# Performance work log

Hardware: AMD Instinct MI355X
Metric: run time of the kernel (lower is better)

Reference implementation:

```python
import jax, jax.numpy as jnp
import numpy as np

N = 50000   # nodes
E = 640000  # edges
IN = 256    # in_dim
H = 128     # hidden
OUT = 40    # out_dim
EPS = 1e-5  # BatchNorm eps


def setup_inputs() -> dict:
    key = jax.random.key(0)
    ks = jax.random.split(key, 14)
    x = jax.random.normal(ks[0], (N, IN), jnp.float32)
    edge_index = jax.random.randint(ks[1], (2, E), 0, N)
    def lin(k, fan_in, shape):
        return jax.random.normal(k, shape, jnp.float32) / np.float32(np.sqrt(fan_in))
    return {
        "x": x,
        "edge_index": edge_index,
        # block 0 (256 -> 128, has res_proj)
        "W0": lin(ks[2], IN, (IN, H)),
        "b0": jnp.zeros((H,), jnp.float32),
        "g0": jnp.ones((H,), jnp.float32),
        "be0": jnp.zeros((H,), jnp.float32),
        "pW": lin(ks[3], IN, (IN, H)),
        "pb": jnp.zeros((H,), jnp.float32),
        # block 1 (128 -> 128, identity residual)
        "W1": lin(ks[4], H, (H, H)),
        "b1": jnp.zeros((H,), jnp.float32),
        "g1": jnp.ones((H,), jnp.float32),
        "be1": jnp.zeros((H,), jnp.float32),
        # head
        "hW": lin(ks[5], H, (H, OUT)),
        "hb": jnp.zeros((OUT,), jnp.float32),
    }


def _gcn_conv(x, W, b, edge_index):
    """GCNConv(improved=True): x' = D^-1/2 (A + 2I) D^-1/2 (x W) + b."""
    h = x @ W  # [N, dout]
    row, col = edge_index[0], edge_index[1]  # source -> target
    # degree of A + 2I (edge_weight = 1, self-loop fill = 2.0)
    deg = jnp.zeros((N,), h.dtype).at[col].add(1.0) + 2.0
    dis = jax.lax.rsqrt(deg)  # deg > 0 always (self-loops)
    norm = dis[row] * dis[col]  # [E]
    # neighbor aggregation: scatter-add normalized messages to targets
    agg = jnp.zeros_like(h).at[col].add(norm[:, None] * h[row])
    # self-loop contribution with weight 2.0
    agg = agg + (2.0 * dis * dis)[:, None] * h
    return agg + b


def _bn(x, gamma, beta):
    # batch statistics (training-mode BatchNorm math), biased variance
    m = jnp.mean(x, axis=0)
    v = jnp.mean(jnp.square(x - m), axis=0)
    return (x - m) * jax.lax.rsqrt(v + EPS) * gamma + beta


def reference(x, edge_index, W0, b0, g0, be0, pW, pb, W1, b1, g1, be1, hW, hb):
    # block 0: conv -> bn -> relu -> (+ res_proj(x))
    out = jax.nn.relu(_bn(_gcn_conv(x, W0, b0, edge_index), g0, be0))
    x1 = out + (x @ pW + pb)
    # block 1: conv -> bn -> relu -> (+ identity)
    out = jax.nn.relu(_bn(_gcn_conv(x1, W1, b1, edge_index), g1, be1))
    x2 = out + x1
    return x2 @ hW + hb  # [N, OUT]
```

## Files before the change

kernel.cpp:

```cpp
#include <hip/hip_runtime.h>

#define H 128
#define IN_DIM 256
#define OUT_DIM 40
#define EPS 1e-5f

typedef unsigned short ushortT;
typedef __attribute__((ext_vector_type(8))) short bf16x8;
typedef __attribute__((ext_vector_type(4))) float f32x4;

static __device__ __forceinline__ ushortT f2bf(float f) {
    union { float f; unsigned u; } v; v.f = f;
    unsigned r = v.u + 0x7FFF + ((v.u >> 16) & 1);
    return (ushortT)(r >> 16);
}
static __device__ __forceinline__ unsigned pk2(float a, float b) {
    return (unsigned)f2bf(a) | ((unsigned)f2bf(b) << 16);
}
static __device__ __forceinline__ float bflo(unsigned v) {
    union { unsigned u; float f; } t; t.u = v << 16; return t.f;
}
static __device__ __forceinline__ float bfhi(unsigned v) {
    union { unsigned u; float f; } t; t.u = v & 0xFFFF0000u; return t.f;
}


__global__ __launch_bounds__(256) void count_kernel(const int* __restrict__ ei, int E, int* __restrict__ cnt) {
    int e = blockIdx.x * 256 + threadIdx.x;
    if (e < E) atomicAdd(&cnt[ei[E + e]], 1);
}

__global__ __launch_bounds__(256) void scan_block_sum(const int* __restrict__ cnt, int* __restrict__ bsum,
                                                      float* __restrict__ dis, int N) {
    __shared__ int s[256];
    int i = blockIdx.x * 256 + threadIdx.x;
    int v = (i < N) ? cnt[i] : 0;
    if (i < N) dis[i] = rsqrtf((float)v + 2.0f);
    s[threadIdx.x] = v;
    __syncthreads();
    for (int o = 128; o > 0; o >>= 1) {
        if (threadIdx.x < o) s[threadIdx.x] += s[threadIdx.x + o];
        __syncthreads();
    }
    if (threadIdx.x == 0) bsum[blockIdx.x] = s[0];
}

__global__ void scan_tops(const int* __restrict__ bsum, int* __restrict__ boff, int* __restrict__ rowptrN, int nb) {
    __shared__ int s[256];
    int t = threadIdx.x;
    int v = (t < nb) ? bsum[t] : 0;
    s[t] = v;
    __syncthreads();
    for (int o = 1; o < 256; o <<= 1) {
        int u = (t >= o) ? s[t - o] : 0;
        __syncthreads();
        s[t] += u;
        __syncthreads();
    }
    if (t < nb) boff[t] = s[t] - v;
    if (t == 255) *rowptrN = s[255];
}

__global__ __launch_bounds__(256) void scan_final(const int* __restrict__ cnt, const int* __restrict__ boff,
                                                  int* __restrict__ rowptr, int* __restrict__ cursor, int N) {
    __shared__ int s[256];
    int t = threadIdx.x;
    int i = blockIdx.x * 256 + t;
    int v = (i < N) ? cnt[i] : 0;
    s[t] = v;
    __syncthreads();
    for (int o = 1; o < 256; o <<= 1) {
        int u = (t >= o) ? s[t - o] : 0;
        __syncthreads();
        s[t] += u;
        __syncthreads();
    }
    if (i < N) {
        int e = boff[blockIdx.x] + s[t] - v;
        rowptr[i] = e;
        cursor[i] = e;
    }
}

__global__ __launch_bounds__(256) void fill_xcd(const int* __restrict__ ei, int E, int nper,
                                                int* __restrict__ cursor, int* __restrict__ eidx) {
    int xcd = blockIdx.x & 7;
    int nchunk = gridDim.x >> 3;
    int chunk = blockIdx.x >> 3;
    int csz = (E + nchunk - 1) / nchunk;
    int beg = chunk * csz;
    int end = min(E, beg + csz);
    for (int e = beg + (int)threadIdx.x; e < end; e += 256) {
        int c = ei[E + e];
        if (c / nper == xcd) {
            int slot = atomicAdd(&cursor[c], 1);
            eidx[slot] = ei[e];
        }
    }
}


__global__ __launch_bounds__(256) void prep_weights(const float* __restrict__ W0, const float* __restrict__ pW,
                                                    const float* __restrict__ W1, const float* __restrict__ hW,
                                                    ushortT* __restrict__ Wt0, ushortT* __restrict__ WtP,
                                                    ushortT* __restrict__ Wt1, ushortT* __restrict__ WtH) {
    int i = blockIdx.x * 256 + threadIdx.x;
    if (i < 32768) { int n = i >> 8, k = i & 255; Wt0[i] = f2bf(W0[k * 128 + n]); WtP[i] = f2bf(pW[k * 128 + n]); }
    if (i < 16384) { int n = i >> 7, k = i & 127; Wt1[i] = f2bf(W1[k * 128 + n]); }
    if (i < 6144)  { int n = i >> 7, k = i & 127; WtH[i] = (n < OUT_DIM) ? f2bf(hW[k * OUT_DIM + n]) : (ushortT)0; }
}


__global__ __launch_bounds__(512) void mgemm0(const float* __restrict__ X,
                                              const ushortT* __restrict__ Wt0,
                                              const ushortT* __restrict__ WtP,
                                              const float* __restrict__ pb,
                                              ushortT* __restrict__ Oh,
                                              ushortT* __restrict__ Op,
                                              int N) {
    __shared__ __align__(16) ushortT S[17408];
    int tid = threadIdx.x;
    int brow = blockIdx.x * 64;

#pragma unroll
    for (int i = 0; i < 8; ++i) {
        int idx = i * 512 + tid;
        int row = idx >> 6, c4 = idx & 63;
        int gr = brow + row;
        float4 v = make_float4(0.f, 0.f, 0.f, 0.f);
        if (gr < N) v = *(const float4*)&X[(size_t)gr * IN_DIM + c4 * 4];
        uint2 p;
        p.x = pk2(v.x, v.y);
        p.y = pk2(v.z, v.w);
        *(uint2*)&S[row * 264 + c4 * 4] = p;
    }
    __syncthreads();

    int w = tid >> 6, lane = tid & 63;
    int lm = lane & 15, lk = lane >> 4;
    int mat = w >> 2;
    int colbase = (w & 3) * 32;
    const ushortT* Wt = mat ? WtP : Wt0;

    f32x4 acc[4][2];
#pragma unroll
    for (int mt = 0; mt < 4; ++mt)
#pragma unroll
        for (int nt = 0; nt < 2; ++nt) acc[mt][nt] = (f32x4)0.f;

#pragma unroll
    for (int kc = 0; kc < 2; ++kc) {
        bf16x8 breg[2][4];
#pragma unroll
        for (int nt = 0; nt < 2; ++nt)
#pragma unroll
            for (int ks = 0; ks < 4; ++ks)
                breg[nt][ks] = *(const bf16x8*)&Wt[(size_t)(colbase + nt * 16 + lm) * IN_DIM + kc * 128 + ks * 32 + lk * 8];
#pragma unroll
        for (int ks = 0; ks < 4; ++ks) {
            bf16x8 af[4];
#pragma unroll
            for (int mt = 0; mt < 4; ++mt)
                af[mt] = *(const bf16x8*)&S[(mt * 16 + lm) * 264 + kc * 128 + ks * 32 + lk * 8];
#pragma unroll
            for (int nt = 0; nt < 2; ++nt)
#pragma unroll
                for (int mt = 0; mt < 4; ++mt)
                    acc[mt][nt] = __builtin_amdgcn_mfma_f32_16x16x32_bf16(af[mt], breg[nt][ks], acc[mt][nt], 0, 0, 0);
        }
    }

    float bb[2] = {0.f, 0.f};
    if (mat) {
        bb[0] = pb[colbase + lm];
        bb[1] = pb[colbase + 16 + lm];
    }
    __syncthreads();
#pragma unroll
    for (int mt = 0; mt < 4; ++mt)
#pragma unroll
        for (int nt = 0; nt < 2; ++nt) {
            int col = colbase + nt * 16 + lm;
#pragma unroll
            for (int j = 0; j < 4; ++j) {
                int row = mt * 16 + lk * 4 + j;
                S[mat * 8704 + row * 136 + col] = f2bf(acc[mt][nt][j] + bb[nt]);
            }
        }
    __syncthreads();
#pragma unroll
    for (int i = 0; i < 4; ++i) {
        int idx = i * 512 + tid;
        int m2 = idx >> 10;
        int rem = idx & 1023;
        int row = rem >> 4, colq = rem & 15;
        int gr = brow + row;
        if (gr < N) {
            uint4 v = *(const uint4*)&S[m2 * 8704 + row * 136 + colq * 8];
            ushortT* O = m2 ? Op : Oh;
            *(uint4*)&O[(size_t)gr * 128 + colq * 8] = v;
        }
    }
}


__global__ __launch_bounds__(512) void mgemm1_fused(const uint4* __restrict__ aggb,
                                                    const uint4* __restrict__ projb,
                                                    const float* __restrict__ stats,
                                                    const float* __restrict__ g,
                                                    const float* __restrict__ be,
                                                    const ushortT* __restrict__ Wt1,
                                                    ushortT* __restrict__ O,
                                                    uint4* __restrict__ x1b,
                                                    int N) {
    __shared__ __align__(16) ushortT S[17408];
    __shared__ float sc[128], sh[128];
    int tid = threadIdx.x;
    int brow = blockIdx.x * 128;

    if (tid < 128) {
        float mean = stats[tid] / (float)N;
        float var = stats[128 + tid] / (float)N - mean * mean;
        float inv = rsqrtf(var + EPS);
        float s = g[tid] * inv;
        sc[tid] = s;
        sh[tid] = be[tid] - mean * s;
    }
    __syncthreads();

#pragma unroll
    for (int i = 0; i < 4; ++i) {
        int idx = i * 512 + tid;
        int row = idx >> 4, q = idx & 15;
        int gr = brow + row;
        uint4 a = make_uint4(0u, 0u, 0u, 0u), p = a;
        if (gr < N) {
            size_t gidx = (size_t)gr * 16 + q;
            a = aggb[gidx];
            p = projb[gidx];
        }
        int ch = q * 8;
        float v0 = fmaxf(fmaf(bflo(a.x), sc[ch + 0], sh[ch + 0]), 0.f) + bflo(p.x);
        float v1 = fmaxf(fmaf(bfhi(a.x), sc[ch + 1], sh[ch + 1]), 0.f) + bfhi(p.x);
        float v2 = fmaxf(fmaf(bflo(a.y), sc[ch + 2], sh[ch + 2]), 0.f) + bflo(p.y);
        float v3 = fmaxf(fmaf(bfhi(a.y), sc[ch + 3], sh[ch + 3]), 0.f) + bfhi(p.y);
        float v4 = fmaxf(fmaf(bflo(a.z), sc[ch + 4], sh[ch + 4]), 0.f) + bflo(p.z);
        float v5 = fmaxf(fmaf(bfhi(a.z), sc[ch + 5], sh[ch + 5]), 0.f) + bfhi(p.z);
        float v6 = fmaxf(fmaf(bflo(a.w), sc[ch + 6], sh[ch + 6]), 0.f) + bflo(p.w);
        float v7 = fmaxf(fmaf(bfhi(a.w), sc[ch + 7], sh[ch + 7]), 0.f) + bfhi(p.w);
        uint4 pv;
        pv.x = pk2(v0, v1);
        pv.y = pk2(v2, v3);
        pv.z = pk2(v4, v5);
        pv.w = pk2(v6, v7);
        *(uint4*)&S[row * 136 + q * 8] = pv;
        if (gr < N) x1b[(size_t)gr * 16 + q] = pv;
    }
    __syncthreads();

    int w = tid >> 6, lane = tid & 63;
    int lm = lane & 15, lk = lane >> 4;
    int rh = (w >> 2) * 64;
    int colbase = (w & 3) * 32;

    bf16x8 breg[2][4];
#pragma unroll
    for (int nt = 0; nt < 2; ++nt)
#pragma unroll
        for (int ks = 0; ks < 4; ++ks)
            breg[nt][ks] = *(const bf16x8*)&Wt1[(size_t)(colbase + nt * 16 + lm) * H + ks * 32 + lk * 8];

    f32x4 acc[4][2];
#pragma unroll
    for (int mt = 0; mt < 4; ++mt)
#pragma unroll
        for (int nt = 0; nt < 2; ++nt) acc[mt][nt] = (f32x4)0.f;

#pragma unroll
    for (int ks = 0; ks < 4; ++ks) {
        bf16x8 af[4];
#pragma unroll
        for (int mt = 0; mt < 4; ++mt)
            af[mt] = *(const bf16x8*)&S[(rh + mt * 16 + lm) * 136 + ks * 32 + lk * 8];
#pragma unroll
        for (int nt = 0; nt < 2; ++nt)
#pragma unroll
            for (int mt = 0; mt < 4; ++mt)
                acc[mt][nt] = __builtin_amdgcn_mfma_f32_16x16x32_bf16(af[mt], breg[nt][ks], acc[mt][nt], 0, 0, 0);
    }

    __syncthreads();
#pragma unroll
    for (int mt = 0; mt < 4; ++mt)
#pragma unroll
        for (int nt = 0; nt < 2; ++nt) {
            int col = colbase + nt * 16 + lm;
#pragma unroll
            for (int j = 0; j < 4; ++j) {
                int row = rh + mt * 16 + lk * 4 + j;
                S[row * 136 + col] = f2bf(acc[mt][nt][j]);
            }
        }
    __syncthreads();
#pragma unroll
    for (int i = 0; i < 4; ++i) {
        int idx = i * 512 + tid;
        int row = idx >> 4, colq = idx & 15;
        int gr = brow + row;
        if (gr < N) {
            uint4 v = *(const uint4*)&S[row * 136 + colq * 8];
            *(uint4*)&O[(size_t)gr * 128 + colq * 8] = v;
        }
    }
}


__global__ __launch_bounds__(256) void aggregate_bf(const ushortT* __restrict__ h,
                                                    const int* __restrict__ rowptr,
                                                    const int* __restrict__ eidx,
                                                    const float* __restrict__ dis,
                                                    ushortT* __restrict__ aggb, int N) {
    int n = blockIdx.x * 4 + (threadIdx.x >> 6);
    int lane = threadIdx.x & 63;
    if (n >= N) return;
    int beg = rowptr[n], end = rowptr[n + 1];
    float dn = dis[n];
    const unsigned* h1 = (const unsigned*)h;
    float a0x = 0.f, a0y = 0.f, a1x = 0.f, a1y = 0.f;
    float a2x = 0.f, a2y = 0.f, a3x = 0.f, a3y = 0.f;
    int p = beg;
    for (; p + 3 < end; p += 4) {
        int s0 = eidx[p], s1 = eidx[p + 1], s2 = eidx[p + 2], s3 = eidx[p + 3];
        float n0 = dis[s0] * dn, n1 = dis[s1] * dn, n2 = dis[s2] * dn, n3 = dis[s3] * dn;
        unsigned v0 = h1[(size_t)s0 * 64 + lane];
        unsigned v1 = h1[(size_t)s1 * 64 + lane];
        unsigned v2 = h1[(size_t)s2 * 64 + lane];
        unsigned v3 = h1[(size_t)s3 * 64 + lane];
        a0x = fmaf(n0, bflo(v0), a0x); a0y = fmaf(n0, bfhi(v0), a0y);
        a1x = fmaf(n1, bflo(v1), a1x); a1y = fmaf(n1, bfhi(v1), a1y);
        a2x = fmaf(n2, bflo(v2), a2x); a2y = fmaf(n2, bfhi(v2), a2y);
        a3x = fmaf(n3, bflo(v3), a3x); a3y = fmaf(n3, bfhi(v3), a3y);
    }
    for (; p < end; ++p) {
        int s0 = eidx[p];
        float n0 = dis[s0] * dn;
        unsigned v0 = h1[(size_t)s0 * 64 + lane];
        a0x = fmaf(n0, bflo(v0), a0x); a0y = fmaf(n0, bfhi(v0), a0y);
    }
    {
        unsigned v = h1[(size_t)n * 64 + lane];
        float sw = 2.f * dn * dn;
        a0x = fmaf(sw, bflo(v), a0x); a0y = fmaf(sw, bfhi(v), a0y);
    }
    float rx = (a0x + a1x) + (a2x + a3x);
    float ry = (a0y + a1y) + (a2y + a3y);
    ((unsigned*)aggb)[(size_t)n * 64 + lane] = pk2(rx, ry);
}


__global__ __launch_bounds__(256) void stats_bf(const unsigned* __restrict__ v, int totalU,
                                                float* __restrict__ sums) {
    int tid = blockIdx.x * 256 + threadIdx.x;
    int stride = gridDim.x * 256;
    float sx = 0.f, sy = 0.f, qx = 0.f, qy = 0.f;
    for (int i = tid; i < totalU; i += stride) {
        unsigned u = v[i];
        float a = bflo(u), b = bfhi(u);
        sx += a; sy += b;
        qx = fmaf(a, a, qx); qy = fmaf(b, b, qy);
    }
    __shared__ float l0[256], l1[256], l2[256], l3[256];
    int t = threadIdx.x;
    l0[t] = sx; l1[t] = sy; l2[t] = qx; l3[t] = qy;
    __syncthreads();
    if (t < 64) {
        sx = (l0[t] + l0[t + 64]) + (l0[t + 128] + l0[t + 192]);
        sy = (l1[t] + l1[t + 64]) + (l1[t + 128] + l1[t + 192]);
        qx = (l2[t] + l2[t + 64]) + (l2[t + 128] + l2[t + 192]);
        qy = (l3[t] + l3[t + 64]) + (l3[t + 128] + l3[t + 192]);
        atomicAdd(&sums[2 * t], sx);
        atomicAdd(&sums[2 * t + 1], sy);
        atomicAdd(&sums[128 + 2 * t], qx);
        atomicAdd(&sums[128 + 2 * t + 1], qy);
    }
}


__global__ __launch_bounds__(256) void head_fused(const uint4* __restrict__ aggb,
                                                  const uint4* __restrict__ x1b,
                                                  const float* __restrict__ stats,
                                                  const float* __restrict__ g,
                                                  const float* __restrict__ be,
                                                  const ushortT* __restrict__ WtH,
                                                  const float* __restrict__ hb,
                                                  float* __restrict__ out, int N) {
    __shared__ __align__(16) ushortT As[64][136];
    __shared__ __align__(16) ushortT Bs[48][136];
    __shared__ float sc[128], sh[128];

    int tid = threadIdx.x;
    int brow = blockIdx.x * 64;
    int w = tid >> 6, lane = tid & 63;
    int lm = lane & 15, lk = lane >> 4;

    if (tid < 128) {
        float mean = stats[tid] / (float)N;
        float var = stats[128 + tid] / (float)N - mean * mean;
        float inv = rsqrtf(var + EPS);
        float s = g[tid] * inv;
        sc[tid] = s;
        sh[tid] = be[tid] - mean * s;
    }
    if (tid < 192) {
        int row = tid >> 2, q = tid & 3;
        const uint4* src = (const uint4*)&WtH[(size_t)row * H + q * 32];
        uint4 a = src[0], b = src[1], c = src[2], d = src[3];
        uint4* dst = (uint4*)&Bs[row][q * 32];
        dst[0] = a; dst[1] = b; dst[2] = c; dst[3] = d;
    }
    __syncthreads();
#pragma unroll
    for (int k = 0; k < 4; ++k) {
        int idx = k * 256 + tid;
        int row = idx >> 4, colq = idx & 15;
        int gr = brow + row;
        uint4 a = make_uint4(0u, 0u, 0u, 0u), x = a;
        if (gr < N) {
            size_t gidx = (size_t)brow * 16 + idx;
            a = aggb[gidx];
            x = x1b[gidx];
        }
        int ch = colq * 8;
        float v0 = fmaxf(fmaf(bflo(a.x), sc[ch + 0], sh[ch + 0]), 0.f) + bflo(x.x);
        float v1 = fmaxf(fmaf(bfhi(a.x), sc[ch + 1], sh[ch + 1]), 0.f) + bfhi(x.x);
        float v2 = fmaxf(fmaf(bflo(a.y), sc[ch + 2], sh[ch + 2]), 0.f) + bflo(x.y);
        float v3 = fmaxf(fmaf(bfhi(a.y), sc[ch + 3], sh[ch + 3]), 0.f) + bfhi(x.y);
        float v4 = fmaxf(fmaf(bflo(a.z), sc[ch + 4], sh[ch + 4]), 0.f) + bflo(x.z);
        float v5 = fmaxf(fmaf(bfhi(a.z), sc[ch + 5], sh[ch + 5]), 0.f) + bfhi(x.z);
        float v6 = fmaxf(fmaf(bflo(a.w), sc[ch + 6], sh[ch + 6]), 0.f) + bflo(x.w);
        float v7 = fmaxf(fmaf(bfhi(a.w), sc[ch + 7], sh[ch + 7]), 0.f) + bfhi(x.w);
        uint4 pv;
        pv.x = pk2(v0, v1);
        pv.y = pk2(v2, v3);
        pv.z = pk2(v4, v5);
        pv.w = pk2(v6, v7);
        *(uint4*)&As[row][colq * 8] = pv;
    }
    __syncthreads();

    f32x4 acc[3];
#pragma unroll
    for (int nt = 0; nt < 3; ++nt) acc[nt] = (f32x4)0.f;
#pragma unroll
    for (int ks = 0; ks < 4; ++ks) {
        bf16x8 a = *(const bf16x8*)&As[w * 16 + lm][ks * 32 + lk * 8];
#pragma unroll
        for (int nt = 0; nt < 3; ++nt) {
            bf16x8 b = *(const bf16x8*)&Bs[nt * 16 + lm][ks * 32 + lk * 8];
            acc[nt] = __builtin_amdgcn_mfma_f32_16x16x32_bf16(a, b, acc[nt], 0, 0, 0);
        }
    }
#pragma unroll
    for (int nt = 0; nt < 3; ++nt) {
        int col = nt * 16 + lm;
        if (col < OUT_DIM) {
            float bbv = hb[col];
#pragma unroll
            for (int j = 0; j < 4; ++j) {
                int r = brow + w * 16 + lk * 4 + j;
                if (r < N) out[(size_t)r * OUT_DIM + col] = acc[nt][j] + bbv;
            }
        }
    }
}


extern "C" void kernel_launch(void* const* d_in, const int* in_sizes, int n_in,
                              void* d_out, int out_size, void* d_ws, size_t ws_size,
                              hipStream_t stream) {
    const float* x   = (const float*)d_in[0];
    const int*   ei  = (const int*)d_in[1];
    const float* W0  = (const float*)d_in[2];
    const float* g0  = (const float*)d_in[4];
    const float* be0 = (const float*)d_in[5];
    const float* pW  = (const float*)d_in[6];
    const float* pb  = (const float*)d_in[7];
    const float* W1  = (const float*)d_in[8];
    const float* g1  = (const float*)d_in[10];
    const float* be1 = (const float*)d_in[11];
    const float* hW  = (const float*)d_in[12];
    const float* hb  = (const float*)d_in[13];
    float* out = (float*)d_out;

    int N = in_sizes[0] / IN_DIM;
    int E = in_sizes[1] / 2;
    size_t NH = (size_t)N * H;

    ushortT* hb16   = (ushortT*)d_ws;
    ushortT* aggb   = hb16 + NH;
    ushortT* projb  = aggb + NH;
    ushortT* x1b    = projb + NH;
    float*   dis    = (float*)(x1b + NH);
    int*     cnt    = (int*)(dis + N);
    int*     rowptr = cnt + N;
    int*     cursor = rowptr + (N + 1);
    int*     eidx   = cursor + N;
    float*   stats  = (float*)(eidx + E);
    ushortT* Wt0    = (ushortT*)(stats + 256);
    ushortT* WtP    = Wt0 + 128 * 256;
    ushortT* Wt1    = WtP + 128 * 256;
    ushortT* WtH    = Wt1 + 128 * 128;
    int*     bsum   = (int*)(WtH + 48 * 128);
    int*     boff   = bsum + 256;

    int gE = (E + 255) / 256;
    int nb = (N + 255) / 256;
    int g64 = (N + 63) / 64;
    int g128 = (N + 127) / 128;
    int gAgg = (N + 3) / 4;

    hipMemsetAsync(cnt, 0, (size_t)N * sizeof(int), stream);
    prep_weights<<<128, 256, 0, stream>>>(W0, pW, W1, hW, Wt0, WtP, Wt1, WtH);
    count_kernel<<<gE, 256, 0, stream>>>(ei, E, cnt);
    scan_block_sum<<<nb, 256, 0, stream>>>(cnt, bsum, dis, N);
    scan_tops<<<1, 256, 0, stream>>>(bsum, boff, &rowptr[N], nb);
    scan_final<<<nb, 256, 0, stream>>>(cnt, boff, rowptr, cursor, N);
    fill_xcd<<<2048, 256, 0, stream>>>(ei, E, (N + 7) / 8, cursor, eidx);

    mgemm0<<<g64, 512, 0, stream>>>(x, Wt0, WtP, pb, hb16, projb, N);
    aggregate_bf<<<gAgg, 256, 0, stream>>>(hb16, rowptr, eidx, dis, aggb, N);
    hipMemsetAsync(stats, 0, 256 * sizeof(float), stream);
    stats_bf<<<256, 256, 0, stream>>>((const unsigned*)aggb, (int)(NH / 2), stats);

    mgemm1_fused<<<g128, 512, 0, stream>>>((const uint4*)aggb, (const uint4*)projb, stats, g0, be0,
                                           Wt1, hb16, (uint4*)x1b, N);
    aggregate_bf<<<gAgg, 256, 0, stream>>>(hb16, rowptr, eidx, dis, aggb, N);
    hipMemsetAsync(stats, 0, 256 * sizeof(float), stream);
    stats_bf<<<256, 256, 0, stream>>>((const unsigned*)aggb, (int)(NH / 2), stats);

    head_fused<<<g64, 256, 0, stream>>>((const uint4*)aggb, (const uint4*)x1b, stats, g1, be1,
                                        WtH, hb, out, N);
}
```

Baseline: 262.3 us.

## Precompute edge norms in CSR records, persist layer-0 GEMM, fold memsets

New measurement: 261.6 us. About the same (-0.3%).

```diff
diff --git a/kernel.cpp b/kernel.cpp
--- a/kernel.cpp
+++ b/kernel.cpp
@@ -23,19 +23,35 @@
 static __device__ __forceinline__ float bfhi(unsigned v) {
     union { unsigned u; float f; } t; t.u = v & 0xFFFF0000u; return t.f;
 }
-
-
-__global__ __launch_bounds__(256) void count_kernel(const int* __restrict__ ei, int E, int* __restrict__ cnt) {
-    int e = blockIdx.x * 256 + threadIdx.x;
-    if (e < E) atomicAdd(&cnt[ei[E + e]], 1);
+static __device__ __forceinline__ float i2f(int v) {
+    union { int i; float f; } t; t.i = v; return t.f;
+}
+static __device__ __forceinline__ int f2i(float v) {
+    union { float f; int i; } t; t.f = v; return t.i;
+}
+
+
+__global__ __launch_bounds__(256) void count_xcd(const int* __restrict__ ei, int E, int nper,
+                                                 int* __restrict__ cnt) {
+    int xcd = blockIdx.x & 7;
+    int nchunk = gridDim.x >> 3;
+    int chunk = blockIdx.x >> 3;
+    int csz = (E + nchunk - 1) / nchunk;
+    int beg = chunk * csz;
+    int end = min(E, beg + csz);
+    for (int e = beg + (int)threadIdx.x; e < end; e += 256) {
+        int c = ei[E + e];
+        if (c / nper == xcd) atomicAdd(&cnt[c], 1);
+    }
 }
 
 __global__ __launch_bounds__(256) void scan_block_sum(const int* __restrict__ cnt, int* __restrict__ bsum,
                                                       float* __restrict__ dis, int N) {
     __shared__ int s[256];
     int i = blockIdx.x * 256 + threadIdx.x;
-    int v = (i < N) ? cnt[i] : 0;
-    if (i < N) dis[i] = rsqrtf((float)v + 2.0f);
+    int c = (i < N) ? cnt[i] : -1;
+    int v = (i < N) ? c + 1 : 0;
+    if (i < N) dis[i] = rsqrtf((float)c + 2.0f);
     s[threadIdx.x] = v;
     __syncthreads();
     for (int o = 128; o > 0; o >>= 1) {
@@ -62,11 +78,13 @@
 }
 
 __global__ __launch_bounds__(256) void scan_final(const int* __restrict__ cnt, const int* __restrict__ boff,
-                                                  int* __restrict__ rowptr, int* __restrict__ cursor, int N) {
+                                                  const float* __restrict__ dis,
+                                                  int* __restrict__ rowptr, int* __restrict__ cursor,
+                                                  int2* __restrict__ recs, int N) {
     __shared__ int s[256];
     int t = threadIdx.x;
     int i = blockIdx.x * 256 + t;
-    int v = (i < N) ? cnt[i] : 0;
+    int v = (i < N) ? cnt[i] + 1 : 0;
     s[t] = v;
     __syncthreads();
     for (int o = 1; o < 256; o <<= 1) {
@@ -78,12 +96,16 @@
     if (i < N) {
         int e = boff[blockIdx.x] + s[t] - v;
         rowptr[i] = e;
-        cursor[i] = e;
+        cursor[i] = e + 1;
+        float d = dis[i];
+        int2 r; r.x = i; r.y = f2i(2.0f * d * d);
+        recs[e] = r;
     }
 }
 
 __global__ __launch_bounds__(256) void fill_xcd(const int* __restrict__ ei, int E, int nper,
-                                                int* __restrict__ cursor, int* __restrict__ eidx) {
+                                                const float* __restrict__ dis,
+                                                int* __restrict__ cursor, int2* __restrict__ recs) {
     int xcd = blockIdx.x & 7;
     int nchunk = gridDim.x >> 3;
     int chunk = blockIdx.x >> 3;
@@ -93,8 +115,10 @@
     for (int e = beg + (int)threadIdx.x; e < end; e += 256) {
         int c = ei[E + e];
         if (c / nper == xcd) {
+            int r = ei[e];
             int slot = atomicAdd(&cursor[c], 1);
-            eidx[slot] = ei[e];
+            int2 rec; rec.x = r; rec.y = f2i(dis[r] * dis[c]);
+            recs[slot] = rec;
         }
     }
 }
@@ -103,102 +127,116 @@
 __global__ __launch_bounds__(256) void prep_weights(const float* __restrict__ W0, const float* __restrict__ pW,
                                                     const float* __restrict__ W1, const float* __restrict__ hW,
                                                     ushortT* __restrict__ Wt0, ushortT* __restrict__ WtP,
-                                                    ushortT* __restrict__ Wt1, ushortT* __restrict__ WtH) {
+                                                    ushortT* __restrict__ Wt1, ushortT* __restrict__ WtH,
+                                                    int* __restrict__ cnt, float* __restrict__ stats, int N) {
     int i = blockIdx.x * 256 + threadIdx.x;
     if (i < 32768) { int n = i >> 8, k = i & 255; Wt0[i] = f2bf(W0[k * 128 + n]); WtP[i] = f2bf(pW[k * 128 + n]); }
     if (i < 16384) { int n = i >> 7, k = i & 127; Wt1[i] = f2bf(W1[k * 128 + n]); }
     if (i < 6144)  { int n = i >> 7, k = i & 127; WtH[i] = (n < OUT_DIM) ? f2bf(hW[k * OUT_DIM + n]) : (ushortT)0; }
-}
-
-
-__global__ __launch_bounds__(512) void mgemm0(const float* __restrict__ X,
-                                              const ushortT* __restrict__ Wt0,
-                                              const ushortT* __restrict__ WtP,
-                                              const float* __restrict__ pb,
-                                              ushortT* __restrict__ Oh,
-                                              ushortT* __restrict__ Op,
-                                              int N) {
-    __shared__ __align__(16) ushortT S[17408];
+    if (i < N) cnt[i] = 0;
+    if (i < 512) stats[i] = 0.f;
+}
+
+
+static __device__ __forceinline__ void g0_loads(const float* __restrict__ X, int brow, int kc,
+                                                int tid, int N, float4 pf[4]) {
+#pragma unroll
+    for (int i = 0; i < 4; ++i) {
+        int idx = i * 512 + tid;
+        int row = idx >> 5, c4 = idx & 31;
+        int gr = brow + row;
+        pf[i] = make_float4(0.f, 0.f, 0.f, 0.f);
+        if (gr < N) pf[i] = *(const float4*)&X[(size_t)gr * IN_DIM + kc * 128 + c4 * 4];
+    }
+}
+static __device__ __forceinline__ void g0_write(ushortT* __restrict__ Sbuf, int tid, const float4 pf[4]) {
+#pragma unroll
+    for (int i = 0; i < 4; ++i) {
+        int idx = i * 512 + tid;
+        int row = idx >> 5, c4 = idx & 31;
+        uint2 p;
+        p.x = pk2(pf[i].x, pf[i].y);
+        p.y = pk2(pf[i].z, pf[i].w);
+        *(uint2*)&Sbuf[row * 136 + c4 * 4] = p;
+    }
+}
+
+__global__ __launch_bounds__(512) void mgemm0p(const float* __restrict__ X,
+                                               const ushortT* __restrict__ Wt0,
+                                               const ushortT* __restrict__ WtP,
+                                               const float* __restrict__ pb,
+                                               ushortT* __restrict__ Oh,
+                                               ushortT* __restrict__ Op,
+                                               int N, int ntiles) {
+    __shared__ __align__(16) ushortT S[2][64 * 136];
     int tid = threadIdx.x;
-    int brow = blockIdx.x * 64;
-
-#pragma unroll
-    for (int i = 0; i < 8; ++i) {
-        int idx = i * 512 + tid;
-        int row = idx >> 6, c4 = idx & 63;
-        int gr = brow + row;
-        float4 v = make_float4(0.f, 0.f, 0.f, 0.f);
-        if (gr < N) v = *(const float4*)&X[(size_t)gr * IN_DIM + c4 * 4];
-        uint2 p;
-        p.x = pk2(v.x, v.y);
-        p.y = pk2(v.z, v.w);
-        *(uint2*)&S[row * 264 + c4 * 4] = p;
-    }
-    __syncthreads();
-
     int w = tid >> 6, lane = tid & 63;
     int lm = lane & 15, lk = lane >> 4;
     int mat = w >> 2;
     int colbase = (w & 3) * 32;
     const ushortT* Wt = mat ? WtP : Wt0;
 
+    bf16x8 breg[2][8];
+#pragma unroll
+    for (int nt = 0; nt < 2; ++nt)
+#pragma unroll
+        for (int kk = 0; kk < 8; ++kk)
+            breg[nt][kk] = *(const bf16x8*)&Wt[(size_t)(colbase + nt * 16 + lm) * IN_DIM + kk * 32 + lk * 8];
+    float bb[2];
+    bb[0] = mat ? pb[colbase + lm] : 0.f;
+    bb[1] = mat ? pb[colbase + 16 + lm] : 0.f;
+    ushortT* O = mat ? Op : Oh;
+
+    int bid = blockIdx.x, G = gridDim.x;
+    int T = (ntiles - 1 - bid) / G + 1;
+    int U = 2 * T;
+
+    float4 pf[4];
+    g0_loads(X, bid * 64, 0, tid, N, pf);
+    g0_write(S[0], tid, pf);
+
     f32x4 acc[4][2];
 #pragma unroll
     for (int mt = 0; mt < 4; ++mt)
 #pragma unroll
         for (int nt = 0; nt < 2; ++nt) acc[mt][nt] = (f32x4)0.f;
 
-#pragma unroll
-    for (int kc = 0; kc < 2; ++kc) {
-        bf16x8 breg[2][4];
-#pragma unroll
-        for (int nt = 0; nt < 2; ++nt)
-#pragma unroll
-            for (int ks = 0; ks < 4; ++ks)
-                breg[nt][ks] = *(const bf16x8*)&Wt[(size_t)(colbase + nt * 16 + lm) * IN_DIM + kc * 128 + ks * 32 + lk * 8];
-#pragma unroll
-        for (int ks = 0; ks < 4; ++ks) {
+    for (int u = 0; u < U; ++u) {
+        __syncthreads();
+        if (u + 1 < U) {
+            int t1 = bid + ((u + 1) >> 1) * G;
+            g0_loads(X, t1 * 64, (u + 1) & 1, tid, N, pf);
+        }
+        int kc = u & 1;
+        const ushortT* Sc = S[u & 1];
+#pragma unroll
+        for (int kk = 0; kk < 4; ++kk) {
             bf16x8 af[4];
 #pragma unroll
             for (int mt = 0; mt < 4; ++mt)
-                af[mt] = *(const bf16x8*)&S[(mt * 16 + lm) * 264 + kc * 128 + ks * 32 + lk * 8];
+                af[mt] = *(const bf16x8*)&Sc[(mt * 16 + lm) * 136 + kk * 32 + lk * 8];
 #pragma unroll
             for (int nt = 0; nt < 2; ++nt)
 #pragma unroll
                 for (int mt = 0; mt < 4; ++mt)
-                    acc[mt][nt] = __builtin_amdgcn_mfma_f32_16x16x32_bf16(af[mt], breg[nt][ks], acc[mt][nt], 0, 0, 0);
-        }
-    }
-
-    float bb[2] = {0.f, 0.f};
-    if (mat) {
-        bb[0] = pb[colbase + lm];
-        bb[1] = pb[colbase + 16 + lm];
-    }
-    __syncthreads();
-#pragma unroll
-    for (int mt = 0; mt < 4; ++mt)
-#pragma unroll
-        for (int nt = 0; nt < 2; ++nt) {
-            int col = colbase + nt * 16 + lm;
-#pragma unroll
-            for (int j = 0; j < 4; ++j) {
-                int row = mt * 16 + lk * 4 + j;
-                S[mat * 8704 + row * 136 + col] = f2bf(acc[mt][nt][j] + bb[nt]);
-            }
-        }
-    __syncthreads();
-#pragma unroll
-    for (int i = 0; i < 4; ++i) {
-        int idx = i * 512 + tid;
-        int m2 = idx >> 10;
-        int rem = idx & 1023;
-        int row = rem >> 4, colq = rem & 15;
-        int gr = brow + row;
-        if (gr < N) {
-            uint4 v = *(const uint4*)&S[m2 * 8704 + row * 136 + colq * 8];
-            ushortT* O = m2 ? Op : Oh;
-            *(uint4*)&O[(size_t)gr * 128 + colq * 8] = v;
+                    acc[mt][nt] = __builtin_amdgcn_mfma_f32_16x16x32_bf16(af[mt], breg[nt][kc * 4 + kk], acc[mt][nt], 0, 0, 0);
+        }
+        if (u + 1 < U) g0_write(S[(u + 1) & 1], tid, pf);
+        if (kc == 1) {
+            int t = bid + (u >> 1) * G;
+            int brow = t * 64;
+#pragma unroll
+            for (int mt = 0; mt < 4; ++mt)
+#pragma unroll
+                for (int nt = 0; nt < 2; ++nt) {
+                    int col = colbase + nt * 16 + lm;
+#pragma unroll
+                    for (int j = 0; j < 4; ++j) {
+                        int r = brow + mt * 16 + lk * 4 + j;
+                        if (r < N) O[(size_t)r * 128 + col] = f2bf(acc[mt][nt][j] + bb[nt]);
+                    }
+                    acc[mt][nt] = (f32x4)0.f;
+                }
         }
     }
 }
@@ -315,46 +353,48 @@
 }
 
 
-__global__ __launch_bounds__(256) void aggregate_bf(const ushortT* __restrict__ h,
-                                                    const int* __restrict__ rowptr,
-                                                    const int* __restrict__ eidx,
-                                                    const float* __restrict__ dis,
-                                                    ushortT* __restrict__ aggb, int N) {
+__global__ __launch_bounds__(256) void aggregate_rec(const ushortT* __restrict__ h,
+                                                     const int* __restrict__ rowptr,
+                                                     const int2* __restrict__ recs,
+                                                     ushortT* __restrict__ aggb, int N) {
     int n = blockIdx.x * 4 + (threadIdx.x >> 6);
+    if (n >= N) return;
     int lane = threadIdx.x & 63;
-    if (n >= N) return;
+    int half = lane >> 5, cl = lane & 31;
     int beg = rowptr[n], end = rowptr[n + 1];
-    float dn = dis[n];
-    const unsigned* h1 = (const unsigned*)h;
-    float a0x = 0.f, a0y = 0.f, a1x = 0.f, a1y = 0.f;
-    float a2x = 0.f, a2y = 0.f, a3x = 0.f, a3y = 0.f;
-    int p = beg;
-    for (; p + 3 < end; p += 4) {
-        int s0 = eidx[p], s1 = eidx[p + 1], s2 = eidx[p + 2], s3 = eidx[p + 3];
-        float n0 = dis[s0] * dn, n1 = dis[s1] * dn, n2 = dis[s2] * dn, n3 = dis[s3] * dn;
-        unsigned v0 = h1[(size_t)s0 * 64 + lane];
-        unsigned v1 = h1[(size_t)s1 * 64 + lane];
-        unsigned v2 = h1[(size_t)s2 * 64 + lane];
-        unsigned v3 = h1[(size_t)s3 * 64 + lane];
-        a0x = fmaf(n0, bflo(v0), a0x); a0y = fmaf(n0, bfhi(v0), a0y);
-        a1x = fmaf(n1, bflo(v1), a1x); a1y = fmaf(n1, bfhi(v1), a1y);
-        a2x = fmaf(n2, bflo(v2), a2x); a2y = fmaf(n2, bfhi(v2), a2y);
-        a3x = fmaf(n3, bflo(v3), a3x); a3y = fmaf(n3, bfhi(v3), a3y);
-    }
-    for (; p < end; ++p) {
-        int s0 = eidx[p];
-        float n0 = dis[s0] * dn;
-        unsigned v0 = h1[(size_t)s0 * 64 + lane];
-        a0x = fmaf(n0, bflo(v0), a0x); a0y = fmaf(n0, bfhi(v0), a0y);
-    }
-    {
-        unsigned v = h1[(size_t)n * 64 + lane];
-        float sw = 2.f * dn * dn;
-        a0x = fmaf(sw, bflo(v), a0x); a0y = fmaf(sw, bfhi(v), a0y);
-    }
-    float rx = (a0x + a1x) + (a2x + a3x);
-    float ry = (a0y + a1y) + (a2y + a3y);
-    ((unsigned*)aggb)[(size_t)n * 64 + lane] = pk2(rx, ry);
+    const uint2* h2 = (const uint2*)h;
+    float a0 = 0.f, a1 = 0.f, a2 = 0.f, a3 = 0.f;
+    float b0 = 0.f, b1 = 0.f, b2 = 0.f, b3 = 0.f;
+    int idx = beg + half;
+    for (; idx + 2 < end; idx += 4) {
+        int2 r0 = recs[idx];
+        int2 r1 = recs[idx + 2];
+        uint2 v0 = h2[(size_t)r0.x * 32 + cl];
+        uint2 v1 = h2[(size_t)r1.x * 32 + cl];
+        float n0 = i2f(r0.y), n1 = i2f(r1.y);
+        a0 = fmaf(n0, bflo(v0.x), a0); a1 = fmaf(n0, bfhi(v0.x), a1);
+        a2 = fmaf(n0, bflo(v0.y), a2); a3 = fmaf(n0, bfhi(v0.y), a3);
+        b0 = fmaf(n1, bflo(v1.x), b0); b1 = fmaf(n1, bfhi(v1.x), b1);
+        b2 = fmaf(n1, bflo(v1.y), b2); b3 = fmaf(n1, bfhi(v1.y), b3);
+    }
+    if (idx < end) {
+        int2 r0 = recs[idx];
+        uint2 v0 = h2[(size_t)r0.x * 32 + cl];
+        float n0 = i2f(r0.y);
+        a0 = fmaf(n0, bflo(v0.x), a0); a1 = fmaf(n0, bfhi(v0.x), a1);
+        a2 = fmaf(n0, bflo(v0.y), a2); a3 = fmaf(n0, bfhi(v0.y), a3);
+    }
+    a0 += b0; a1 += b1; a2 += b2; a3 += b3;
+    a0 += __shfl_xor(a0, 32);
+    a1 += __shfl_xor(a1, 32);
+    a2 += __shfl_xor(a2, 32);
+    a3 += __shfl_xor(a3, 32);
+    if (half == 0) {
+        uint2 o;
+        o.x = pk2(a0, a1);
+        o.y = pk2(a2, a3);
+        ((uint2*)aggb)[(size_t)n * 32 + cl] = o;
+    }
 }
 
 
@@ -504,40 +544,40 @@
     int*     cnt    = (int*)(dis + N);
     int*     rowptr = cnt + N;
     int*     cursor = rowptr + (N + 1);
-    int*     eidx   = cursor + N;
-    float*   stats  = (float*)(eidx + E);
-    ushortT* Wt0    = (ushortT*)(stats + 256);
+    int2*    recs   = (int2*)(cursor + N);
+    float*   stats  = (float*)(recs + (E + N));
+    ushortT* Wt0    = (ushortT*)(stats + 512);
     ushortT* WtP    = Wt0 + 128 * 256;
     ushortT* Wt1    = WtP + 128 * 256;
     ushortT* WtH    = Wt1 + 128 * 128;
     int*     bsum   = (int*)(WtH + 48 * 128);
     int*     boff   = bsum + 256;
-
-    int gE = (E + 255) / 256;
+    float*   stats0 = stats;
+    float*   stats1 = stats + 256;
+
     int nb = (N + 255) / 256;
     int g64 = (N + 63) / 64;
     int g128 = (N + 127) / 128;
     int gAgg = (N + 3) / 4;
-
-    hipMemsetAsync(cnt, 0, (size_t)N * sizeof(int), stream);
-    prep_weights<<<128, 256, 0, stream>>>(W0, pW, W1, hW, Wt0, WtP, Wt1, WtH);
-    count_kernel<<<gE, 256, 0, stream>>>(ei, E, cnt);
+    int ntiles = g64;
+    int gPersist = (ntiles + 1) / 2;
+
+    prep_weights<<<196, 256, 0, stream>>>(W0, pW, W1, hW, Wt0, WtP, Wt1, WtH, cnt, stats, N);
+    count_xcd<<<2048, 256, 0, stream>>>(ei, E, (N + 7) / 8, cnt);
     scan_block_sum<<<nb, 256, 0, stream>>>(cnt, bsum, dis, N);
     scan_tops<<<1, 256, 0, stream>>>(bsum, boff, &rowptr[N], nb);
-    scan_final<<<nb, 256, 0, stream>>>(cnt, boff, rowptr, cursor, N);
-    fill_xcd<<<2048, 256, 0, stream>>>(ei, E, (N + 7) / 8, cursor, eidx);
-
-    mgemm0<<<g64, 512, 0, stream>>>(x, Wt0, WtP, pb, hb16, projb, N);
-    aggregate_bf<<<gAgg, 256, 0, stream>>>(hb16, rowptr, eidx, dis, aggb, N);
-    hipMemsetAsync(stats, 0, 256 * sizeof(float), stream);
-    stats_bf<<<256, 256, 0, stream>>>((const unsigned*)aggb, (int)(NH / 2), stats);
-
-    mgemm1_fused<<<g128, 512, 0, stream>>>((const uint4*)aggb, (const uint4*)projb, stats, g0, be0,
+    scan_final<<<nb, 256, 0, stream>>>(cnt, boff, dis, rowptr, cursor, recs, N);
+    fill_xcd<<<2048, 256, 0, stream>>>(ei, E, (N + 7) / 8, dis, cursor, recs);
+
+    mgemm0p<<<gPersist, 512, 0, stream>>>(x, Wt0, WtP, pb, hb16, projb, N, ntiles);
+    aggregate_rec<<<gAgg, 256, 0, stream>>>(hb16, rowptr, recs, aggb, N);
+    stats_bf<<<256, 256, 0, stream>>>((const unsigned*)aggb, (int)(NH / 2), stats0);
+
+    mgemm1_fused<<<g128, 512, 0, stream>>>((const uint4*)aggb, (const uint4*)projb, stats0, g0, be0,
                                            Wt1, hb16, (uint4*)x1b, N);
-    aggregate_bf<<<gAgg, 256, 0, stream>>>(hb16, rowptr, eidx, dis, aggb, N);
-    hipMemsetAsync(stats, 0, 256 * sizeof(float), stream);
-    stats_bf<<<256, 256, 0, stream>>>((const unsigned*)aggb, (int)(NH / 2), stats);
-
-    head_fused<<<g64, 256, 0, stream>>>((const uint4*)aggb, (const uint4*)x1b, stats, g1, be1,
+    aggregate_rec<<<gAgg, 256, 0, stream>>>(hb16, rowptr, recs, aggb, N);
+    stats_bf<<<256, 256, 0, stream>>>((const unsigned*)aggb, (int)(NH / 2), stats1);
+
+    head_fused<<<g64, 256, 0, stream>>>((const uint4*)aggb, (const uint4*)x1b, stats1, g1, be1,
                                         WtH, hb, out, N);
 }
```
